# Kernel optimization log

Hardware: AMD Instinct MI355X
Metric: run time of the kernel (lower is better)

## Reference

```python
import jax, jax.numpy as jnp
import numpy as np

N = 8192; S = 32; EMB = 256; NH = 8; HD = EMB // NH; NT = 4; K = 2; L = 2; E = 131072
IN_DIMS = [128, 64, 32, 16]; COUNTS = [4096, 2048, 1024, 1024]
BETA = 1.0; TEMPER = 1.0; SLOPE = 0.2; LN_EPS = 1e-5


def setup_inputs() -> dict:
    key = jax.random.key(0)
    ks = iter(jax.random.split(key, 64))
    def nrm(shape, scale=1.0):
        return jax.random.normal(next(ks), shape, jnp.float32) * scale
    inp = {}
    for i, (d, c) in enumerate(zip(IN_DIMS, COUNTS)):
        inp[f"feat{i}"] = nrm((c, d))
        inp[f"Wfc{i}"] = nrm((d, EMB), d ** -0.5)
        inp[f"bfc{i}"] = nrm((EMB,), 0.01)
    inp["type_emb"] = nrm((NT, NT))
    inp["Wgcn"] = nrm((K, EMB, EMB), EMB ** -0.5)
    inp["bgcn"] = nrm((K, EMB), 0.01)
    inp["Wre"] = nrm((K, NT, NT), NT ** -0.5)
    inp["bre"] = nrm((K, NT), 0.01)
    inp["wtre"] = jnp.ones((K, NT), jnp.float32)
    inp["Wl"] = nrm((L, EMB, EMB), EMB ** -0.5)
    inp["Wr"] = nrm((L, EMB, EMB), EMB ** -0.5)
    inp["al"] = nrm((L, HD), HD ** -0.5)
    inp["ar"] = nrm((L, HD), HD ** -0.5)
    inp["Wrs"] = nrm((L, NT, NT * NH), NT ** -0.5)
    inp["Wrt"] = nrm((L, NT, NT * NH), NT ** -0.5)
    inp["Wfin"] = nrm((L, EMB, EMB), EMB ** -0.5)
    inp["ln_g"] = jnp.ones((L, EMB), jnp.float32)
    inp["ln_b"] = jnp.zeros((L, EMB), jnp.float32)
    inp["src"] = jax.random.randint(next(ks), (E,), 0, N)
    inp["dst"] = jax.random.randint(next(ks), (E,), 0, N)
    inp["node_type"] = jnp.concatenate([jnp.full((c,), t, jnp.int32) for t, c in enumerate(COUNTS)])
    inp["seqs"] = jax.random.randint(next(ks), (N, S), 0, N)
    return inp


def _l2n(x):
    return x / jnp.maximum(jnp.linalg.norm(x, axis=1, keepdims=True), 1e-12)


def _ln(x, g, b):
    m = x.mean(-1, keepdims=True)
    v = ((x - m) ** 2).mean(-1, keepdims=True)
    return (x - m) * jax.lax.rsqrt(v + LN_EPS) * g + b


def _agt(h, rh, Wl_, Wr_, al_, ar_, Wrs_, Wrt_, Wfin_, g_, b_):
    B, Sq, _ = h.shape
    fl = (h @ Wl_).reshape(B, Sq, NH, HD).transpose(0, 2, 1, 3)  # [B,NH,S,HD]
    fr = (h @ Wr_).reshape(B, Sq, NH, HD).transpose(0, 2, 1, 3)
    sl = jnp.einsum('bhsd,d->bhs', jax.nn.leaky_relu(fl, SLOPE), al_)
    sr = jnp.einsum('bhsd,d->bhs', jax.nn.leaky_relu(fr, SLOPE), ar_)
    score = sl[:, :, :, None] + sr[:, :, None, :]  # [B,NH,S,S]
    rk = (rh @ Wrs_).reshape(B, Sq, NH, NT).transpose(0, 2, 1, 3)  # [B,NH,S,NT]
    rq = (rh @ Wrt_).reshape(B, Sq, NH, NT).transpose(0, 2, 1, 3)
    score = score + BETA * jnp.einsum('bhir,bhjr->bhij', rk, rq)
    attn = jax.nn.softmax(score / TEMPER, axis=-1)
    ctx = jnp.einsum('bhij,bhjd->bhid', attn, fr)
    h_sa = ctx.transpose(0, 2, 1, 3).reshape(B, Sq, EMB)
    return _ln(h + h_sa @ Wfin_, g_, b_)


def reference(feat0, feat1, feat2, feat3, Wfc0, bfc0, Wfc1, bfc1, Wfc2, bfc2, Wfc3, bfc3,
              type_emb, Wgcn, bgcn, Wre, bre, wtre, Wl, Wr, al, ar, Wrs, Wrt, Wfin, ln_g, ln_b,
              src, dst, node_type, seqs):
    feats = [feat0, feat1, feat2, feat3]
    Wfcs = [Wfc0, Wfc1, Wfc2, Wfc3]
    bfcs = [bfc0, bfc1, bfc2, bfc3]
    gh = jnp.concatenate([f @ W + b for f, W, b in zip(feats, Wfcs, bfcs)], axis=0)  # [N,EMB]
    Nn = gh.shape[0]
    loop = jnp.arange(Nn, dtype=src.dtype)  # self-loops (graph.add_self_loop)
    src_f = jnp.concatenate([src, loop]); dst_f = jnp.concatenate([dst, loop])
    ones = jnp.ones(src_f.shape[0], jnp.float32)
    outdeg = jnp.clip(jax.ops.segment_sum(ones, src_f, num_segments=Nn), 1.0)
    indeg = jnp.clip(jax.ops.segment_sum(ones, dst_f, num_segments=Nn), 1.0)
    n_out = outdeg ** -0.5; n_in = indeg ** -0.5
    ret = [_l2n(gh)]
    R = type_emb[node_type]  # [N,NT]
    for k in range(K):
        # GraphConv, norm='both', relu
        x = (gh * n_out[:, None]) @ Wgcn[k]
        gh = jax.nn.relu(jax.ops.segment_sum(x[src_f], dst_f, num_segments=Nn) * n_in[:, None] + bgcn[k])
        # REConv: left norm, weight, per-node type scale, scatter-sum, right norm, bias, relu
        r = ((R * n_out[:, None]) @ Wre[k]) * wtre[k][node_type][:, None]
        R = jax.nn.relu(jax.ops.segment_sum(r[src_f], dst_f, num_segments=Nn) * n_in[:, None] + bre[k])
    h = gh[seqs]   # [N,S,EMB]
    rh = R[seqs]   # [N,S,NT]
    for l in range(L):
        h = _agt(h, rh, Wl[l], Wr[l], al[l], ar[l], Wrs[l], Wrt[l], Wfin[l], ln_g[l], ln_b[l])
        ret.append(_l2n(h[:, 0, :]))
    return jnp.concatenate(ret, axis=1)  # [N, EMB*(1+L)]
```

## Files before the change

kernel.cpp:

```cpp
#include <hip/hip_runtime.h>
#include <hip/hip_bf16.h>
#include <cstdint>
#include <cstddef>

typedef unsigned short ushortT;
typedef unsigned int uintT;

using bf16x8 = __attribute__((ext_vector_type(8))) short;
using f32x4  = __attribute__((ext_vector_type(4))) float;

static constexpr int NN  = 8192;
static constexpr int EE  = 131072;
static constexpr float SLOPE  = 0.2f;
static constexpr float LN_EPS = 1e-5f;

#define DEVI __device__ __forceinline__

DEVI float red32(float v) {
  #pragma unroll
  for (int m = 16; m >= 1; m >>= 1) v += __shfl_xor(v, m, 64);
  return v;
}
DEVI float red64(float v) {
  #pragma unroll
  for (int m = 32; m >= 1; m >>= 1) v += __shfl_xor(v, m, 64);
  return v;
}
DEVI float max32(float v) {
  #pragma unroll
  for (int m = 16; m >= 1; m >>= 1) v = fmaxf(v, __shfl_xor(v, m, 64));
  return v;
}
DEVI float blo(uintT u) { union { uintT i; float f; } c; c.i = u << 16; return c.f; }
DEVI float bhi(uintT u) { union { uintT i; float f; } c; c.i = u & 0xffff0000u; return c.f; }
DEVI float b2f(ushortT u) { union { uintT i; float f; } c; c.i = ((uintT)u) << 16; return c.f; }
DEVI ushortT f2bu(float f) {
  __hip_bfloat16 h = __float2bfloat16(f);
  return *reinterpret_cast<ushortT*>(&h);
}
DEVI void storeC(float* p, float v) { *p = v; }
DEVI void storeC(ushortT* p, float v) { *p = f2bu(v); }

__global__ __launch_bounds__(256) void fc_kernel(
    const float* __restrict__ f0, const float* __restrict__ f1,
    const float* __restrict__ f2, const float* __restrict__ f3,
    const float* __restrict__ w0, const float* __restrict__ w1,
    const float* __restrict__ w2, const float* __restrict__ w3,
    const float* __restrict__ b0, const float* __restrict__ b1,
    const float* __restrict__ b2, const float* __restrict__ b3,
    float* __restrict__ gh, float* __restrict__ out)
{
  const int nb = blockIdx.x * 32;
  const int t  = threadIdx.x;
  int base, D;
  const float *F, *W, *Bv;
  if (nb < 4096)      { base = 0;    D = 128; F = f0; W = w0; Bv = b0; }
  else if (nb < 6144) { base = 4096; D = 64;  F = f1; W = w1; Bv = b1; }
  else if (nb < 7168) { base = 6144; D = 32;  F = f2; W = w2; Bv = b2; }
  else                { base = 7168; D = 16;  F = f3; W = w3; Bv = b3; }

  __shared__ float Fs[32 * 128];
  __shared__ float red[32][4];
  __shared__ float nrm[32];

  const int total = 32 * D;
  for (int i = t; i < total; i += 256) Fs[i] = F[(size_t)(nb - base) * D + i];
  __syncthreads();

  float acc[32];
  #pragma unroll
  for (int r = 0; r < 32; ++r) acc[r] = Bv[t];
  for (int d = 0; d < D; ++d) {
    float w = W[(size_t)d * 256 + t];
    #pragma unroll
    for (int r = 0; r < 32; ++r) acc[r] = fmaf(Fs[r * D + d], w, acc[r]);
  }

  const int lane = t & 63, wid = t >> 6;
  #pragma unroll
  for (int r = 0; r < 32; ++r) {
    float v = acc[r] * acc[r];
    for (int o = 32; o > 0; o >>= 1) v += __shfl_down(v, o, 64);
    if (lane == 0) red[r][wid] = v;
  }
  __syncthreads();
  if (t < 32) {
    float s = red[t][0] + red[t][1] + red[t][2] + red[t][3];
    nrm[t] = 1.0f / fmaxf(sqrtf(s), 1e-12f);
  }
  __syncthreads();
  #pragma unroll
  for (int r = 0; r < 32; ++r) {
    gh[(size_t)(nb + r) * 256 + t]  = acc[r];
    out[(size_t)(nb + r) * 768 + t] = acc[r] * nrm[r];
  }
}

__global__ __launch_bounds__(256) void zero_counts(int* outc, int* inc) {
  int g = blockIdx.x * 256 + threadIdx.x;
  if (g < NN) outc[g] = 0; else inc[g - NN] = 0;
}
__global__ __launch_bounds__(256) void count_deg(const int* __restrict__ src,
                                                 const int* __restrict__ dst,
                                                 int* outc, int* inc) {
  int g = blockIdx.x * 256 + threadIdx.x;
  atomicAdd(&outc[src[g]], 1);
  atomicAdd(&inc[dst[g]], 1);
}
__global__ __launch_bounds__(256) void norm_kernel(const int* __restrict__ outc,
                                                   const int* __restrict__ inc,
                                                   float* n_out, float* n_in) {
  int g = blockIdx.x * 256 + threadIdx.x;
  n_out[g] = rsqrtf((float)outc[g] + 1.0f);
  n_in[g]  = rsqrtf((float)inc[g] + 1.0f);
}
__global__ __launch_bounds__(1024) void scan_kernel(const int* __restrict__ inc,
                                                    int* __restrict__ offs) {
  __shared__ int sums[1024];
  const int t = threadIdx.x;
  int x[8];
  const int base = t * 8;
  int s = 0;
  #pragma unroll
  for (int i = 0; i < 8; ++i) { int v = inc[base + i] + 1; x[i] = s; s += v; }
  sums[t] = s;
  __syncthreads();
  for (int off = 1; off < 1024; off <<= 1) {
    int a = (t >= off) ? sums[t - off] : 0;
    __syncthreads();
    sums[t] += a;
    __syncthreads();
  }
  const int pre = (t > 0) ? sums[t - 1] : 0;
  #pragma unroll
  for (int i = 0; i < 8; ++i) offs[base + i] = pre + x[i];
  if (t == 1023) offs[NN] = sums[1023];
}
__global__ __launch_bounds__(256) void copy_cur(const int* __restrict__ offs, int* cur) {
  int g = blockIdx.x * 256 + threadIdx.x;
  cur[g] = offs[g];
}
__global__ __launch_bounds__(256) void fill_csr(const int* __restrict__ src,
                                                const int* __restrict__ dst,
                                                int* cur, int* __restrict__ csr) {
  int g = blockIdx.x * 256 + threadIdx.x;
  int s, d;
  if (g < EE) { s = src[g]; d = dst[g]; }
  else        { s = g - EE; d = g - EE; }
  int pos = atomicAdd(&cur[d], 1);
  csr[pos] = s;
}
__global__ __launch_bounds__(256) void init_R(const float* __restrict__ type_emb,
                                              const int* __restrict__ nt,
                                              float* __restrict__ R) {
  int g = blockIdx.x * 256 + threadIdx.x;
  int n = g >> 2, c = g & 3;
  R[g] = type_emb[nt[n] * 4 + c];
}

template<bool ROWSCALE, bool STORE, bool RED, typename CT>
__global__ __launch_bounds__(256) void gemm64_kernel(
    const float* __restrict__ A,
    const float* __restrict__ W,
    const float* __restrict__ rowscale,
    CT* __restrict__ C,
    const float* __restrict__ avec,
    float* __restrict__ SSo)
{
  const int m0 = blockIdx.x * 64;
  const int n0 = blockIdx.y * 64;
  const int t  = threadIdx.x;
  const int tr = t & 15, tc = t >> 4;
  __shared__ alignas(16) float As[32][68];
  __shared__ alignas(16) float Bs[32][68];
  __shared__ float red[64][2];
  float acc[4][4] = {};

  for (int ks = 0; ks < 8; ++ks) {
    const int k0 = ks * 32;
    #pragma unroll
    for (int rep = 0; rep < 8; ++rep) {
      int flat = rep * 256 + t;
      int r = flat >> 5, c = flat & 31;
      As[c][r] = A[(size_t)(m0 + r) * 256 + (k0 + c)];
      int rb = flat >> 6, cb = flat & 63;
      Bs[rb][cb] = W[(size_t)(k0 + rb) * 256 + (n0 + cb)];
    }
    __syncthreads();
    #pragma unroll
    for (int k = 0; k < 32; ++k) {
      const float4 a4 = *reinterpret_cast<const float4*>(&As[k][tr * 4]);
      const float4 b4 = *reinterpret_cast<const float4*>(&Bs[k][tc * 4]);
      const float av[4] = {a4.x, a4.y, a4.z, a4.w};
      const float bv[4] = {b4.x, b4.y, b4.z, b4.w};
      #pragma unroll
      for (int u = 0; u < 4; ++u)
        #pragma unroll
        for (int v = 0; v < 4; ++v)
          acc[u][v] = fmaf(av[u], bv[v], acc[u][v]);
    }
    __syncthreads();
  }

  if constexpr (ROWSCALE) {
    #pragma unroll
    for (int u = 0; u < 4; ++u) {
      float s = rowscale[m0 + tr * 4 + u];
      #pragma unroll
      for (int v = 0; v < 4; ++v) acc[u][v] *= s;
    }
  }
  if constexpr (STORE) {
    #pragma unroll
    for (int u = 0; u < 4; ++u) {
      size_t row = (size_t)(m0 + tr * 4 + u);
      #pragma unroll
      for (int v = 0; v < 4; ++v)
        storeC(&C[row * 256 + (n0 + tc * 4 + v)], acc[u][v]);
    }
  }
  if constexpr (RED) {
    if (t < 128) red[t >> 1][t & 1] = 0.f;
    __syncthreads();
    #pragma unroll
    for (int u = 0; u < 4; ++u) {
      float s = 0.f;
      #pragma unroll
      for (int v = 0; v < 4; ++v) {
        float x = acc[u][v];
        float lr = x > 0.f ? x : SLOPE * x;
        s += lr * avec[(tc * 4 + v) & 31];
      }
      atomicAdd(&red[tr * 4 + u][tc >> 3], s);
    }
    __syncthreads();
    if (t < 128) {
      int r = t >> 1, hh = t & 1;
      SSo[(size_t)(m0 + r) * 8 + blockIdx.y * 2 + hh] = red[r][hh];
    }
  }
}

__global__ __launch_bounds__(256) void mfma_tab_kernel(
    const float* __restrict__ GR1, const float* __restrict__ gh,
    const float* __restrict__ Wfin, const float* __restrict__ Wc2,
    const float* __restrict__ Wcl, const float* __restrict__ Wg2,
    const float* __restrict__ Wgl2,
    ushortT* __restrict__ GWo, ushortT* __restrict__ GW2o,
    ushortT* __restrict__ GWLo, ushortT* __restrict__ GHGo,
    ushortT* __restrict__ GHLo)
{
  const int z = blockIdx.z;
  const float* A = (z < 3) ? GR1 : gh;
  const float* W = (z == 0) ? Wfin : (z == 1) ? Wc2 : (z == 2) ? Wcl
                 : (z == 3) ? Wg2 : Wgl2;
  ushortT* C = (z == 0) ? GWo : (z == 1) ? GW2o : (z == 2) ? GWLo
             : (z == 3) ? GHGo : GHLo;

  const int m0 = blockIdx.x * 64;
  const int n0 = blockIdx.y * 64;
  const int t = threadIdx.x;
  const int w = t >> 6, l = t & 63;
  const int wr = w >> 1, wc = w & 1;
  const int l15 = l & 15, l16 = l >> 4;

  __shared__ alignas(16) ushortT As[64][72];
  __shared__ alignas(16) ushortT Bs[64][72];

  f32x4 acc[2][2];
  #pragma unroll
  for (int mh = 0; mh < 2; ++mh)
    #pragma unroll
    for (int nh = 0; nh < 2; ++nh)
      #pragma unroll
      for (int r = 0; r < 4; ++r) acc[mh][nh][r] = 0.f;

  for (int k0 = 0; k0 < 256; k0 += 64) {
    #pragma unroll
    for (int rep = 0; rep < 16; ++rep) {
      int flat = rep * 256 + t;
      int r = flat >> 6, k = flat & 63;
      As[r][k] = f2bu(A[(size_t)(m0 + r) * 256 + k0 + k]);
    }
    #pragma unroll
    for (int rep = 0; rep < 16; ++rep) {
      int flat = rep * 256 + t;
      int k = flat >> 6, n = flat & 63;
      Bs[n][k] = f2bu(W[(size_t)(k0 + k) * 256 + n0 + n]);
    }
    __syncthreads();
    #pragma unroll
    for (int ks = 0; ks < 2; ++ks) {
      const int kb = ks * 32 + l16 * 8;
      bf16x8 afr[2], bfr[2];
      #pragma unroll
      for (int mh = 0; mh < 2; ++mh)
        afr[mh] = *reinterpret_cast<const bf16x8*>(&As[wr * 32 + mh * 16 + l15][kb]);
      #pragma unroll
      for (int nh = 0; nh < 2; ++nh)
        bfr[nh] = *reinterpret_cast<const bf16x8*>(&Bs[wc * 32 + nh * 16 + l15][kb]);
      #pragma unroll
      for (int mh = 0; mh < 2; ++mh)
        #pragma unroll
        for (int nh = 0; nh < 2; ++nh)
          acc[mh][nh] = __builtin_amdgcn_mfma_f32_16x16x32_bf16(
              afr[mh], bfr[nh], acc[mh][nh], 0, 0, 0);
    }
    __syncthreads();
  }
  #pragma unroll
  for (int mh = 0; mh < 2; ++mh)
    #pragma unroll
    for (int nh = 0; nh < 2; ++nh)
      #pragma unroll
      for (int r = 0; r < 4; ++r) {
        const int row = m0 + wr * 32 + mh * 16 + l16 * 4 + r;
        const int col = n0 + wc * 32 + nh * 16 + l15;
        C[(size_t)row * 256 + col] = f2bu(acc[mh][nh][r]);
      }
}

__global__ __launch_bounds__(256) void agg_kernel(
    const int* __restrict__ offs, const int* __restrict__ csr,
    const float* __restrict__ X, const float* __restrict__ n_in,
    const float* __restrict__ bias, float* __restrict__ ghn)
{
  const int n = blockIdx.x, t = threadIdx.x;
  const int s0 = offs[n], s1 = offs[n + 1];
  float acc = 0.f;
  for (int i = s0; i < s1; ++i) acc += X[(size_t)csr[i] * 256 + t];
  ghn[(size_t)n * 256 + t] = fmaxf(fmaf(acc, n_in[n], bias[t]), 0.f);
}
__global__ __launch_bounds__(256) void re_proj(
    const float* __restrict__ R, const float* __restrict__ n_out,
    const float* __restrict__ Wre, const float* __restrict__ wtre,
    const int* __restrict__ nt, float* __restrict__ rtmp)
{
  int g = blockIdx.x * 256 + threadIdx.x;
  int n = g >> 2, j = g & 3;
  float s = 0.f;
  #pragma unroll
  for (int c = 0; c < 4; ++c) s += R[n * 4 + c] * Wre[c * 4 + j];
  rtmp[g] = s * n_out[n] * wtre[nt[n]];
}
__global__ __launch_bounds__(256) void re_agg(
    const int* __restrict__ offs, const int* __restrict__ csr,
    const float* __restrict__ rtmp, const float* __restrict__ n_in,
    const float* __restrict__ bre, float* __restrict__ Rn)
{
  int g = blockIdx.x * 256 + threadIdx.x;
  int n = g >> 2, j = g & 3;
  float a = 0.f;
  for (int i = offs[n]; i < offs[n + 1]; ++i) a += rtmp[csr[i] * 4 + j];
  Rn[g] = fmaxf(fmaf(a, n_in[n], bre[j]), 0.f);
}
__global__ __launch_bounds__(256) void rkq_kernel(
    const float* __restrict__ R, const float* __restrict__ Wrs,
    const float* __restrict__ Wrt, float* __restrict__ RKQ)
{
  int g = blockIdx.x * 256 + threadIdx.x;
  int n = g >> 7, c = g & 127;
  int which = c >> 5, cc = c & 31;
  const float* Wp = (which == 0) ? Wrs : (which == 1) ? Wrt
                   : (which == 2) ? (Wrs + 128) : (Wrt + 128);
  float s = 0.f;
  #pragma unroll
  for (int r = 0; r < 4; ++r) s += R[n * 4 + r] * Wp[r * 32 + cc];
  RKQ[g] = s;
}

__global__ __launch_bounds__(256) void scale_w_kernel(
    const float* __restrict__ ln_g, const float* __restrict__ Wr2,
    const float* __restrict__ Wl2, float* __restrict__ Wg2,
    float* __restrict__ Wgl2)
{
  int g = blockIdx.x * 256 + threadIdx.x;
  float s = ln_g[g >> 8];
  Wg2[g]  = s * Wr2[g];
  Wgl2[g] = s * Wl2[g];
}
__global__ __launch_bounds__(256) void vec4_kernel(
    const float* __restrict__ ln_g, const float* __restrict__ ln_b,
    const float* __restrict__ Wr2, const float* __restrict__ Wl2,
    float* __restrict__ vecs)
{
  const int which = blockIdx.x, t = threadIdx.x;
  const float* W = (which < 2) ? Wr2 : Wl2;
  const float* s = (which & 1) ? ln_b : ln_g;
  float a = 0.f;
  for (int k = 0; k < 256; ++k) a = fmaf(s[k], W[(size_t)k * 256 + t], a);
  vecs[which * 256 + t] = a;
}

__global__ __launch_bounds__(256) void mega4_kernel(
    const int* __restrict__ seqs,
    const float* __restrict__ gh,
    const ushortT* __restrict__ GW, const ushortT* __restrict__ GW2,
    const ushortT* __restrict__ GWL, const ushortT* __restrict__ GHG,
    const ushortT* __restrict__ GHL,
    const float* __restrict__ SLg, const float* __restrict__ SRg,
    const float* __restrict__ RKQ,
    const float* __restrict__ vecs,
    const float* __restrict__ al2, const float* __restrict__ ar2,
    const float* __restrict__ ln_g, const float* __restrict__ ln_b,
    float* __restrict__ h1r0buf, float* __restrict__ ctx2buf,
    float* __restrict__ out)
{
  __shared__ int idx[32];
  __shared__ alignas(16) ushortT GT[256 * 40];
  __shared__ alignas(16) ushortT PlF[10240];
  __shared__ float SRs[8][32];
  __shared__ float RQs[32][36];
  __shared__ float rk2s[32];
  __shared__ float part[32][4], partq[32][4];
  __shared__ float mu_s[32], rs_s[32];
  __shared__ float SR2s[8][32];
  __shared__ float sl2s[8];
  __shared__ float scp[8][32];
  __shared__ float h1r0s[256];
  __shared__ float wred4[4];
  __shared__ float nrm1s;

  const int b = blockIdx.x, t = threadIdx.x;
  const int h8 = t >> 5, lo = t & 31;
  const int w = t >> 6, l = t & 63;
  const int l15 = l & 15, l16 = l >> 4;

  if (t < 32) idx[t] = seqs[b * 32 + t];
  __syncthreads();

  const float sli = SLg[(size_t)idx[lo] * 8 + h8];
  const float rk0 = RKQ[(size_t)idx[lo] * 128 + h8 * 4 + 0];
  const float rk1 = RKQ[(size_t)idx[lo] * 128 + h8 * 4 + 1];
  const float rk2_ = RKQ[(size_t)idx[lo] * 128 + h8 * 4 + 2];
  const float rk3 = RKQ[(size_t)idx[lo] * 128 + h8 * 4 + 3];

  {
    const uintT* GWu = reinterpret_cast<const uintT*>(GW);
    #pragma unroll
    for (int rep = 0; rep < 16; ++rep) {
      int flat = rep * 256 + t;
      int j = flat >> 7, cp = flat & 127;
      const uintT u = GWu[(size_t)idx[j] * 128 + cp];
      const int rA = 2 * cp;
      const int k = (rA >> 3) & 3;
      const int off = (((j >> 3) ^ k) << 3) + (j & 7);
      GT[rA * 40 + off]       = (ushortT)(u & 0xffffu);
      GT[(rA + 1) * 40 + off] = (ushortT)(u >> 16);
    }
  }
  SRs[h8][lo] = SRg[(size_t)idx[lo] * 8 + h8];
  #pragma unroll
  for (int rep = 0; rep < 4; ++rep) {
    int flat = rep * 256 + t, s3 = flat >> 5, c3 = flat & 31;
    RQs[s3][c3] = RKQ[(size_t)idx[s3] * 128 + 32 + c3];
  }
  if (t < 32) rk2s[t] = RKQ[(size_t)idx[0] * 128 + 64 + t];
  __syncthreads();

  {
    float p1[32];
    float m = -1e30f;
    #pragma unroll
    for (int j = 0; j < 32; ++j) {
      float sc = sli + SRs[h8][j]
               + rk0 * RQs[j][h8 * 4 + 0] + rk1 * RQs[j][h8 * 4 + 1]
               + rk2_ * RQs[j][h8 * 4 + 2] + rk3 * RQs[j][h8 * 4 + 3];
      p1[j] = sc; m = fmaxf(m, sc);
    }
    float sum = 0.f;
    #pragma unroll
    for (int j = 0; j < 32; ++j) { p1[j] = __expf(p1[j] - m); sum += p1[j]; }
    const float inv = 1.f / sum;
    const int row = t;
    const int k = (row >> 3) & 3;
    uintT* pw = reinterpret_cast<uintT*>(PlF);
    #pragma unroll
    for (int q = 0; q < 16; ++q) {
      const int pu = row * 20 + (((q >> 2) ^ k) << 2) + (q & 3);
      pw[pu] = (uintT)f2bu(p1[2 * q] * inv) | ((uintT)f2bu(p1[2 * q + 1] * inv) << 16);
    }
  }
  __syncthreads();

  int irow[2][4];
  #pragma unroll
  for (int mh = 0; mh < 2; ++mh)
    #pragma unroll
    for (int r = 0; r < 4; ++r)
      irow[mh][r] = idx[mh * 16 + l16 * 4 + r];

  bf16x8 af[2][2];
  #pragma unroll
  for (int hh = 0; hh < 2; ++hh) {
    const int h = 2 * w + hh;
    #pragma unroll
    for (int mh = 0; mh < 2; ++mh) {
      const int row = h * 32 + mh * 16 + l15;
      const int k = (row >> 3) & 3;
      af[hh][mh] = *reinterpret_cast<const bf16x8*>(&PlF[row * 40 + ((l16 ^ k) << 3)]);
    }
  }

  f32x4 acc[2][2][2];
  #pragma unroll
  for (int hh = 0; hh < 2; ++hh) {
    const int h = 2 * w + hh;
    bf16x8 bf[2];
    #pragma unroll
    for (int nh = 0; nh < 2; ++nh) {
      const int row = h * 32 + nh * 16 + l15;
      const int k = (row >> 3) & 3;
      bf[nh] = *reinterpret_cast<const bf16x8*>(&GT[row * 40 + ((l16 ^ k) << 3)]);
    }
    #pragma unroll
    for (int mh = 0; mh < 2; ++mh)
      #pragma unroll
      for (int nh = 0; nh < 2; ++nh) {
        f32x4 z = {0.f, 0.f, 0.f, 0.f};
        acc[hh][mh][nh] = __builtin_amdgcn_mfma_f32_16x16x32_bf16(af[hh][mh], bf[nh], z, 0, 0, 0);
      }
  }
  {
    float sum_[2][4], sq_[2][4];
    #pragma unroll
    for (int mh = 0; mh < 2; ++mh)
      #pragma unroll
      for (int r = 0; r < 4; ++r) { sum_[mh][r] = 0.f; sq_[mh][r] = 0.f; }
    #pragma unroll
    for (int hh = 0; hh < 2; ++hh)
      #pragma unroll
      for (int mh = 0; mh < 2; ++mh)
        #pragma unroll
        for (int nh = 0; nh < 2; ++nh) {
          const int col = (2 * w + hh) * 32 + nh * 16 + l15;
          #pragma unroll
          for (int r = 0; r < 4; ++r) {
            float v = acc[hh][mh][nh][r] + gh[(size_t)irow[mh][r] * 256 + col];
            acc[hh][mh][nh][r] = v;
            sum_[mh][r] += v;
            sq_[mh][r] = fmaf(v, v, sq_[mh][r]);
          }
        }
    #pragma unroll
    for (int mh = 0; mh < 2; ++mh)
      #pragma unroll
      for (int r = 0; r < 4; ++r) {
        float s = sum_[mh][r], q = sq_[mh][r];
        #pragma unroll
        for (int m = 8; m >= 1; m >>= 1) {
          s += __shfl_xor(s, m, 64);
          q += __shfl_xor(q, m, 64);
        }
        if (l15 == 0) {
          part[mh * 16 + l16 * 4 + r][w]  = s;
          partq[mh * 16 + l16 * 4 + r][w] = q;
        }
      }
    if (l16 == 0) {
      #pragma unroll
      for (int hh = 0; hh < 2; ++hh)
        #pragma unroll
        for (int nh = 0; nh < 2; ++nh)
          h1r0s[(2 * w + hh) * 32 + nh * 16 + l15] = acc[hh][0][nh][0];
    }
  }
  __syncthreads();

  if (t < 32) {
    float sm = part[t][0] + part[t][1] + part[t][2] + part[t][3];
    float sq = partq[t][0] + partq[t][1] + partq[t][2] + partq[t][3];
    const float m = sm * (1.f / 256.f);
    const float v = fmaxf(sq * (1.f / 256.f) - m * m, 0.f);
    mu_s[t] = m;
    rs_s[t] = rsqrtf(v + LN_EPS);
  }
  __syncthreads();

  {
    const uintT* GW2u = reinterpret_cast<const uintT*>(GW2);
    #pragma unroll
    for (int rep = 0; rep < 16; ++rep) {
      int flat = rep * 256 + t;
      int j = flat >> 7, cp = flat & 127;
      const uintT u = GW2u[(size_t)idx[j] * 128 + cp];
      const int rA = 2 * cp;
      const int k = (rA >> 3) & 3;
      const int off = (((j >> 3) ^ k) << 3) + (j & 7);
      GT[rA * 40 + off]       = (ushortT)(u & 0xffffu);
      GT[(rA + 1) * 40 + off] = (ushortT)(u >> 16);
    }
  }
  #pragma unroll
  for (int rep = 0; rep < 4; ++rep) {
    int flat = rep * 256 + t, s3 = flat >> 5, c3 = flat & 31;
    RQs[s3][c3] = RKQ[(size_t)idx[s3] * 128 + 96 + c3];
  }
  {
    const float mu0 = mu_s[0], rs0 = rs_s[0];
    float hv = fmaf((h1r0s[t] - mu0) * rs0, ln_g[t], ln_b[t]);
    h1r0buf[(size_t)b * 256 + t] = hv;
    float sq = red64(hv * hv);
    h1r0s[t] = hv;
    if ((t & 63) == 0) wred4[t >> 6] = sq;
  }
  {
    float z0 = 0.f;
    #pragma unroll 8
    for (int j = 0; j < 32; ++j)
      z0 = fmaf(b2f(PlF[(h8 * 32) * 40 + j]), b2f(GWL[(size_t)idx[j] * 256 + t]), z0);
    z0 += b2f(GHL[(size_t)idx[0] * 256 + t]);
    const float rs0 = rs_s[0], rm0 = rs_s[0] * mu_s[0];
    const float fl = fmaf(rs0, z0, fmaf(-rm0, vecs[512 + t], vecs[768 + t]));
    float lr = (fl > 0.f ? fl : SLOPE * fl) * al2[lo];
    lr = red32(lr);
    if (lo == 0) sl2s[h8] = lr;
  }
  __syncthreads();

  if (t == 0) nrm1s = 1.f / fmaxf(sqrtf(wred4[0] + wred4[1] + wred4[2] + wred4[3]), 1e-12f);

  {
    f32x4 acc2[2][2][2];
    #pragma unroll
    for (int hh = 0; hh < 2; ++hh) {
      const int h = 2 * w + hh;
      bf16x8 bf[2];
      #pragma unroll
      for (int nh = 0; nh < 2; ++nh) {
        const int row = h * 32 + nh * 16 + l15;
        const int k = (row >> 3) & 3;
        bf[nh] = *reinterpret_cast<const bf16x8*>(&GT[row * 40 + ((l16 ^ k) << 3)]);
      }
      #pragma unroll
      for (int mh = 0; mh < 2; ++mh)
        #pragma unroll
        for (int nh = 0; nh < 2; ++nh) {
          f32x4 z = {0.f, 0.f, 0.f, 0.f};
          acc2[hh][mh][nh] = __builtin_amdgcn_mfma_f32_16x16x32_bf16(af[hh][mh], bf[nh], z, 0, 0, 0);
        }
    }
    float rsv[2][4], rmv[2][4];
    #pragma unroll
    for (int mh = 0; mh < 2; ++mh)
      #pragma unroll
      for (int r = 0; r < 4; ++r) {
        const int row = mh * 16 + l16 * 4 + r;
        rsv[mh][r] = rs_s[row];
        rmv[mh][r] = rsv[mh][r] * mu_s[row];
      }
    float ar2v[2] = { ar2[l15], ar2[16 + l15] };
    float v1c[2][2], v2c[2][2];
    #pragma unroll
    for (int hh = 0; hh < 2; ++hh)
      #pragma unroll
      for (int nh = 0; nh < 2; ++nh) {
        const int col = (2 * w + hh) * 32 + nh * 16 + l15;
        v1c[hh][nh] = vecs[col];
        v2c[hh][nh] = vecs[256 + col];
      }
    float sacc[2][2][4];
    #pragma unroll
    for (int hh = 0; hh < 2; ++hh)
      #pragma unroll
      for (int mh = 0; mh < 2; ++mh)
        #pragma unroll
        for (int r = 0; r < 4; ++r) sacc[hh][mh][r] = 0.f;

    #pragma unroll
    for (int hh = 0; hh < 2; ++hh)
      #pragma unroll
      for (int mh = 0; mh < 2; ++mh)
        #pragma unroll
        for (int nh = 0; nh < 2; ++nh) {
          const int col = (2 * w + hh) * 32 + nh * 16 + l15;
          #pragma unroll
          for (int r = 0; r < 4; ++r) {
            const int row = mh * 16 + l16 * 4 + r;
            float yv = acc2[hh][mh][nh][r] + b2f(GHG[(size_t)irow[mh][r] * 256 + col]);
            float fa = fmaf(rsv[mh][r], yv, fmaf(-rmv[mh][r], v1c[hh][nh], v2c[hh][nh]));
            PlF[row * 268 + col] = f2bu(fa);
            float lr = fa > 0.f ? fa : SLOPE * fa;
            sacc[hh][mh][r] = fmaf(lr, ar2v[nh], sacc[hh][mh][r]);
          }
        }
    #pragma unroll
    for (int hh = 0; hh < 2; ++hh)
      #pragma unroll
      for (int mh = 0; mh < 2; ++mh)
        #pragma unroll
        for (int r = 0; r < 4; ++r) {
          float s = sacc[hh][mh][r];
          #pragma unroll
          for (int m = 8; m >= 1; m >>= 1) s += __shfl_xor(s, m, 64);
          if (l15 == 0) SR2s[2 * w + hh][mh * 16 + l16 * 4 + r] = s;
        }
  }
  __syncthreads();

  {
    float s2 = sl2s[h8] + SR2s[h8][lo]
             + rk2s[h8 * 4 + 0] * RQs[lo][h8 * 4 + 0]
             + rk2s[h8 * 4 + 1] * RQs[lo][h8 * 4 + 1]
             + rk2s[h8 * 4 + 2] * RQs[lo][h8 * 4 + 2]
             + rk2s[h8 * 4 + 3] * RQs[lo][h8 * 4 + 3];
    const float m2 = max32(s2);
    const float e = __expf(s2 - m2);
    const float su = red32(e);
    scp[h8][lo] = e / su;
  }
  __syncthreads();

  {
    float a = 0.f;
    #pragma unroll
    for (int j = 0; j < 32; ++j) a = fmaf(scp[h8][j], b2f(PlF[j * 268 + t]), a);
    ctx2buf[(size_t)b * 256 + t] = a;
  }
  out[(size_t)b * 768 + 256 + t] = h1r0s[t] * nrm1s;
}

__global__ __launch_bounds__(256) void final_ln_kernel(
    const float* __restrict__ A,
    const float* __restrict__ W,
    const float* __restrict__ res,
    const float* __restrict__ lng, const float* __restrict__ lnb,
    float* __restrict__ out)
{
  const int m0 = blockIdx.x * 64;
  const int t  = threadIdx.x;
  const int tr = t & 15, tc = t >> 4;
  __shared__ alignas(16) float As[32][68];
  __shared__ alignas(16) float Bs[32][264];
  __shared__ float red[64][16];
  __shared__ float stat[64];
  float acc[4][16] = {};

  for (int ks = 0; ks < 8; ++ks) {
    const int k0 = ks * 32;
    #pragma unroll
    for (int rep = 0; rep < 8; ++rep) {
      int flat = rep * 256 + t;
      int r = flat >> 5, c = flat & 31;
      As[c][r] = A[(size_t)(m0 + r) * 256 + (k0 + c)];
    }
    #pragma unroll
    for (int rep = 0; rep < 32; ++rep) {
      int flat = rep * 256 + t;
      int rb = flat >> 8, cb = flat & 255;
      Bs[rb][cb] = W[(size_t)(k0 + rb) * 256 + cb];
    }
    __syncthreads();
    #pragma unroll
    for (int k = 0; k < 32; ++k) {
      const float4 a4 = *reinterpret_cast<const float4*>(&As[k][tr * 4]);
      const float av[4] = {a4.x, a4.y, a4.z, a4.w};
      #pragma unroll
      for (int q = 0; q < 4; ++q) {
        const float4 b4 = *reinterpret_cast<const float4*>(&Bs[k][tc * 16 + q * 4]);
        const float bv[4] = {b4.x, b4.y, b4.z, b4.w};
        #pragma unroll
        for (int u = 0; u < 4; ++u)
          #pragma unroll
          for (int v = 0; v < 4; ++v)
            acc[u][q * 4 + v] = fmaf(av[u], bv[v], acc[u][q * 4 + v]);
      }
    }
    __syncthreads();
  }

  int rows[4];
  #pragma unroll
  for (int u = 0; u < 4; ++u) rows[u] = m0 + tr * 4 + u;

  #pragma unroll
  for (int u = 0; u < 4; ++u) {
    const float* rp = &res[(size_t)rows[u] * 256 + tc * 16];
    #pragma unroll
    for (int v = 0; v < 16; ++v) acc[u][v] += rp[v];
  }
  #pragma unroll
  for (int u = 0; u < 4; ++u) {
    float s = 0.f;
    #pragma unroll
    for (int v = 0; v < 16; ++v) s += acc[u][v];
    red[tr * 4 + u][tc] = s;
  }
  __syncthreads();
  if (t < 64) {
    float s = 0.f;
    #pragma unroll
    for (int g = 0; g < 16; ++g) s += red[t][g];
    stat[t] = s * (1.0f / 256.0f);
  }
  __syncthreads();
  float mu[4];
  #pragma unroll
  for (int u = 0; u < 4; ++u) mu[u] = stat[tr * 4 + u];
  #pragma unroll
  for (int u = 0; u < 4; ++u) {
    float s = 0.f;
    #pragma unroll
    for (int v = 0; v < 16; ++v) { float d = acc[u][v] - mu[u]; s += d * d; }
    red[tr * 4 + u][tc] = s;
  }
  __syncthreads();
  if (t < 64) {
    float s = 0.f;
    #pragma unroll
    for (int g = 0; g < 16; ++g) s += red[t][g];
    stat[t] = rsqrtf(s * (1.0f / 256.0f) + LN_EPS);
  }
  __syncthreads();
  float rst[4];
  #pragma unroll
  for (int u = 0; u < 4; ++u) rst[u] = stat[tr * 4 + u];
  #pragma unroll
  for (int u = 0; u < 4; ++u) {
    float s = 0.f;
    #pragma unroll
    for (int v = 0; v < 16; ++v) {
      int col = tc * 16 + v;
      float yv = fmaf((acc[u][v] - mu[u]) * rst[u], lng[col], lnb[col]);
      acc[u][v] = yv;
      s += yv * yv;
    }
    red[tr * 4 + u][tc] = s;
  }
  __syncthreads();
  if (t < 64) {
    float s = 0.f;
    #pragma unroll
    for (int g = 0; g < 16; ++g) s += red[t][g];
    stat[t] = 1.0f / fmaxf(sqrtf(s), 1e-12f);
  }
  __syncthreads();
  #pragma unroll
  for (int u = 0; u < 4; ++u) {
    float rn = stat[tr * 4 + u];
    #pragma unroll
    for (int v = 0; v < 16; ++v)
      out[(size_t)rows[u] * 768 + 512 + tc * 16 + v] = acc[u][v] * rn;
  }
}

extern "C" void kernel_launch(void* const* d_in, const int* in_sizes, int n_in,
                              void* d_out, int out_size, void* d_ws, size_t ws_size,
                              hipStream_t stream)
{
  (void)in_sizes; (void)n_in; (void)out_size; (void)ws_size;

  const float* feat[4]; const float* wfc[4]; const float* bfc[4];
  for (int i = 0; i < 4; ++i) {
    feat[i] = (const float*)d_in[i * 3 + 0];
    wfc[i]  = (const float*)d_in[i * 3 + 1];
    bfc[i]  = (const float*)d_in[i * 3 + 2];
  }
  const float* type_emb = (const float*)d_in[12];
  const float* Wgcn = (const float*)d_in[13];
  const float* bgcn = (const float*)d_in[14];
  const float* Wre  = (const float*)d_in[15];
  const float* bre  = (const float*)d_in[16];
  const float* wtre = (const float*)d_in[17];
  const float* Wl   = (const float*)d_in[18];
  const float* Wr   = (const float*)d_in[19];
  const float* al   = (const float*)d_in[20];
  const float* ar   = (const float*)d_in[21];
  const float* Wrs  = (const float*)d_in[22];
  const float* Wrt  = (const float*)d_in[23];
  const float* Wfin = (const float*)d_in[24];
  const float* ln_g = (const float*)d_in[25];
  const float* ln_b = (const float*)d_in[26];
  const int* src       = (const int*)d_in[27];
  const int* dst       = (const int*)d_in[28];
  const int* node_type = (const int*)d_in[29];
  const int* seqs      = (const int*)d_in[30];
  float* out = (float*)d_out;

  char* p = (char*)d_ws;
  auto take = [&](size_t n) { char* q = p; p += (n + 255) & ~(size_t)255; return q; };
  float* gh    = (float*)take((size_t)NN * 256 * 4);
  float* Xbuf  = (float*)take((size_t)NN * 256 * 4);
  float* GR1   = (float*)take((size_t)NN * 256 * 4);
  float* RKQ   = (float*)take((size_t)NN * 128 * 4);
  float* SLg   = (float*)take((size_t)NN * 8 * 4);
  float* SRg   = (float*)take((size_t)NN * 8 * 4);
  float* n_out = (float*)take((size_t)NN * 4);
  float* n_in_ = (float*)take((size_t)NN * 4);
  int*   outc  = (int*)take((size_t)NN * 4);
  int*   inc   = (int*)take((size_t)NN * 4);
  int*   offs  = (int*)take((size_t)(NN + 1) * 4);
  int*   cur   = (int*)take((size_t)NN * 4);
  int*   csr   = (int*)take((size_t)(EE + NN) * 4);
  float* R     = (float*)take((size_t)NN * 4 * 4);
  float* rtmp  = (float*)take((size_t)NN * 4 * 4);
  ushortT* GW  = (ushortT*)take((size_t)NN * 256 * 2);
  ushortT* GW2 = (ushortT*)take((size_t)NN * 256 * 2);
  ushortT* GWL = (ushortT*)take((size_t)NN * 256 * 2);
  ushortT* GHG = (ushortT*)take((size_t)NN * 256 * 2);
  ushortT* GHL = (ushortT*)take((size_t)NN * 256 * 2);
  float* Wg2   = (float*)take((size_t)65536 * 4);
  float* Wgl2  = (float*)take((size_t)65536 * 4);
  float* Wc2   = (float*)take((size_t)65536 * 4);
  float* Wcl   = (float*)take((size_t)65536 * 4);
  float* vecs  = (float*)take((size_t)4 * 256 * 4);
  float* ctx2buf = Xbuf;
  float* h1r0buf = GR1;

  const float* Wr2 = Wr + 65536;
  const float* Wl2 = Wl + 65536;

  fc_kernel<<<256, 256, 0, stream>>>(feat[0], feat[1], feat[2], feat[3],
                                     wfc[0], wfc[1], wfc[2], wfc[3],
                                     bfc[0], bfc[1], bfc[2], bfc[3], gh, out);
  zero_counts<<<64, 256, 0, stream>>>(outc, inc);
  count_deg<<<512, 256, 0, stream>>>(src, dst, outc, inc);
  norm_kernel<<<32, 256, 0, stream>>>(outc, inc, n_out, n_in_);
  scan_kernel<<<1, 1024, 0, stream>>>(inc, offs);
  copy_cur<<<32, 256, 0, stream>>>(offs, cur);
  fill_csr<<<544, 256, 0, stream>>>(src, dst, cur, csr);
  init_R<<<128, 256, 0, stream>>>(type_emb, node_type, R);

  scale_w_kernel<<<256, 256, 0, stream>>>(ln_g, Wr2, Wl2, Wg2, Wgl2);
  vec4_kernel<<<4, 256, 0, stream>>>(ln_g, ln_b, Wr2, Wl2, vecs);
  gemm64_kernel<false, true, false, float>
      <<<dim3(4, 4), 256, 0, stream>>>(Wfin, Wg2, nullptr, Wc2, nullptr, nullptr);
  gemm64_kernel<false, true, false, float>
      <<<dim3(4, 4), 256, 0, stream>>>(Wfin, Wgl2, nullptr, Wcl, nullptr, nullptr);

  for (int k = 0; k < 2; ++k) {
    gemm64_kernel<true, true, false, float>
        <<<dim3(128, 4), 256, 0, stream>>>(gh, Wgcn + (size_t)k * 65536,
                                           n_out, Xbuf, nullptr, nullptr);
    agg_kernel<<<NN, 256, 0, stream>>>(offs, csr, Xbuf, n_in_, bgcn + k * 256, gh);
    re_proj<<<128, 256, 0, stream>>>(R, n_out, Wre + k * 16, wtre + k * 4, node_type, rtmp);
    re_agg<<<128, 256, 0, stream>>>(offs, csr, rtmp, n_in_, bre + k * 4, R);
  }

  rkq_kernel<<<4096, 256, 0, stream>>>(R, Wrs, Wrt, RKQ);
  gemm64_kernel<false, false, true, float>
      <<<dim3(128, 4), 256, 0, stream>>>(gh, Wl, nullptr, (float*)nullptr, al, SLg);
  gemm64_kernel<false, true, true, float>
      <<<dim3(128, 4), 256, 0, stream>>>(gh, Wr, nullptr, GR1, ar, SRg);
  mfma_tab_kernel<<<dim3(128, 4, 5), 256, 0, stream>>>(
      GR1, gh, Wfin, Wc2, Wcl, Wg2, Wgl2, GW, GW2, GWL, GHG, GHL);

  mega4_kernel<<<NN, 256, 0, stream>>>(seqs, gh, GW, GW2, GWL, GHG, GHL,
                                       SLg, SRg, RKQ, vecs,
                                       al + 32, ar + 32, ln_g, ln_b,
                                       h1r0buf, ctx2buf, out);

  final_ln_kernel<<<128, 256, 0, stream>>>(ctx2buf, Wfin + 65536, h1r0buf,
                                           ln_g + 256, ln_b + 256, out);
}
```

Measured before the change: 627.2 us.

## Compute layer-2 projection per sequence in-kernel instead of precomputed per-node tables

Drops the five precomputed per-node bf16 tables (GW2, GWL, GHG, GHL and the weight products Wc2/Wcl). The mega kernel now builds the layer-1 output tile in shared memory and multiplies it by a transposed, ln_g-scaled bf16 Wr2 through MFMA. The left-score path becomes a direct 256x256 dot product of h1r0 with a bf16 Wl2. gh is read as a bf16 copy. This removes four 8192x256 table GEMMs and the matching gather traffic, but adds per-block MFMA work (32x256x256), weight reads from global or L2, extra bf16 rounding of the residual and of h1, and a serial 256-length loop per thread.

Result: faster. 604.7 us (-3.6%).

```diff
diff --git a/kernel.cpp b/kernel.cpp
--- a/kernel.cpp
+++ b/kernel.cpp
@@ -242,21 +242,9 @@
 }
 
 __global__ __launch_bounds__(256) void mfma_tab_kernel(
-    const float* __restrict__ GR1, const float* __restrict__ gh,
-    const float* __restrict__ Wfin, const float* __restrict__ Wc2,
-    const float* __restrict__ Wcl, const float* __restrict__ Wg2,
-    const float* __restrict__ Wgl2,
-    ushortT* __restrict__ GWo, ushortT* __restrict__ GW2o,
-    ushortT* __restrict__ GWLo, ushortT* __restrict__ GHGo,
-    ushortT* __restrict__ GHLo)
-{
-  const int z = blockIdx.z;
-  const float* A = (z < 3) ? GR1 : gh;
-  const float* W = (z == 0) ? Wfin : (z == 1) ? Wc2 : (z == 2) ? Wcl
-                 : (z == 3) ? Wg2 : Wgl2;
-  ushortT* C = (z == 0) ? GWo : (z == 1) ? GW2o : (z == 2) ? GWLo
-             : (z == 3) ? GHGo : GHLo;
-
+    const float* __restrict__ A, const float* __restrict__ W,
+    ushortT* __restrict__ C)
+{
   const int m0 = blockIdx.x * 64;
   const int n0 = blockIdx.y * 64;
   const int t = threadIdx.x;
@@ -369,46 +357,49 @@
   RKQ[g] = s;
 }
 
-__global__ __launch_bounds__(256) void scale_w_kernel(
-    const float* __restrict__ ln_g, const float* __restrict__ Wr2,
-    const float* __restrict__ Wl2, float* __restrict__ Wg2,
-    float* __restrict__ Wgl2)
-{
-  int g = blockIdx.x * 256 + threadIdx.x;
-  float s = ln_g[g >> 8];
-  Wg2[g]  = s * Wr2[g];
-  Wgl2[g] = s * Wl2[g];
-}
 __global__ __launch_bounds__(256) void vec4_kernel(
     const float* __restrict__ ln_g, const float* __restrict__ ln_b,
-    const float* __restrict__ Wr2, const float* __restrict__ Wl2,
-    float* __restrict__ vecs)
+    const float* __restrict__ Wr2, float* __restrict__ vecs)
 {
   const int which = blockIdx.x, t = threadIdx.x;
-  const float* W = (which < 2) ? Wr2 : Wl2;
   const float* s = (which & 1) ? ln_b : ln_g;
   float a = 0.f;
-  for (int k = 0; k < 256; ++k) a = fmaf(s[k], W[(size_t)k * 256 + t], a);
+  for (int k = 0; k < 256; ++k) a = fmaf(s[k], Wr2[(size_t)k * 256 + t], a);
   vecs[which * 256 + t] = a;
 }
-
-__global__ __launch_bounds__(256) void mega4_kernel(
+__global__ __launch_bounds__(256) void wg2t_kernel(
+    const float* __restrict__ ln_g, const float* __restrict__ Wr2,
+    const float* __restrict__ Wl2,
+    ushortT* __restrict__ Wg2T, ushortT* __restrict__ Wl2b)
+{
+  const int c = blockIdx.x, t = threadIdx.x;
+  Wg2T[(size_t)c * 256 + t] = f2bu(ln_g[t] * Wr2[(size_t)t * 256 + c]);
+  Wl2b[(size_t)c * 256 + t] = f2bu(Wl2[(size_t)c * 256 + t]);
+}
+__global__ __launch_bounds__(256) void ghb_kernel(
+    const float* __restrict__ gh, ushortT* __restrict__ ghb)
+{
+  int g = blockIdx.x * 256 + threadIdx.x;
+  ghb[g] = f2bu(gh[g]);
+}
+
+__global__ __launch_bounds__(256) void mega5_kernel(
     const int* __restrict__ seqs,
-    const float* __restrict__ gh,
-    const ushortT* __restrict__ GW, const ushortT* __restrict__ GW2,
-    const ushortT* __restrict__ GWL, const ushortT* __restrict__ GHG,
-    const ushortT* __restrict__ GHL,
+    const ushortT* __restrict__ ghb,
+    const ushortT* __restrict__ GW,
     const float* __restrict__ SLg, const float* __restrict__ SRg,
     const float* __restrict__ RKQ,
     const float* __restrict__ vecs,
+    const ushortT* __restrict__ Wg2T,
+    const ushortT* __restrict__ Wl2b,
     const float* __restrict__ al2, const float* __restrict__ ar2,
     const float* __restrict__ ln_g, const float* __restrict__ ln_b,
     float* __restrict__ h1r0buf, float* __restrict__ ctx2buf,
     float* __restrict__ out)
 {
   __shared__ int idx[32];
-  __shared__ alignas(16) ushortT GT[256 * 40];
-  __shared__ alignas(16) ushortT PlF[10240];
+  __shared__ alignas(16) ushortT bufA[10240];
+  __shared__ alignas(16) ushortT bufB[10240];
   __shared__ float SRs[8][32];
   __shared__ float RQs[32][36];
   __shared__ float rk2s[32];
@@ -445,8 +436,8 @@
       const int rA = 2 * cp;
       const int k = (rA >> 3) & 3;
       const int off = (((j >> 3) ^ k) << 3) + (j & 7);
-      GT[rA * 40 + off]       = (ushortT)(u & 0xffffu);
-      GT[(rA + 1) * 40 + off] = (ushortT)(u >> 16);
+      bufA[rA * 40 + off]       = (ushortT)(u & 0xffffu);
+      bufA[(rA + 1) * 40 + off] = (ushortT)(u >> 16);
     }
   }
   SRs[h8][lo] = SRg[(size_t)idx[lo] * 8 + h8];
@@ -474,7 +465,7 @@
     const float inv = 1.f / sum;
     const int row = t;
     const int k = (row >> 3) & 3;
-    uintT* pw = reinterpret_cast<uintT*>(PlF);
+    uintT* pw = reinterpret_cast<uintT*>(bufB);
     #pragma unroll
     for (int q = 0; q < 16; ++q) {
       const int pu = row * 20 + (((q >> 2) ^ k) << 2) + (q & 3);
@@ -498,7 +489,7 @@
     for (int mh = 0; mh < 2; ++mh) {
       const int row = h * 32 + mh * 16 + l15;
       const int k = (row >> 3) & 3;
-      af[hh][mh] = *reinterpret_cast<const bf16x8*>(&PlF[row * 40 + ((l16 ^ k) << 3)]);
+      af[hh][mh] = *reinterpret_cast<const bf16x8*>(&bufB[row * 40 + ((l16 ^ k) << 3)]);
     }
   }
 
@@ -511,7 +502,7 @@
     for (int nh = 0; nh < 2; ++nh) {
       const int row = h * 32 + nh * 16 + l15;
       const int k = (row >> 3) & 3;
-      bf[nh] = *reinterpret_cast<const bf16x8*>(&GT[row * 40 + ((l16 ^ k) << 3)]);
+      bf[nh] = *reinterpret_cast<const bf16x8*>(&bufA[row * 40 + ((l16 ^ k) << 3)]);
     }
     #pragma unroll
     for (int mh = 0; mh < 2; ++mh)
@@ -536,7 +527,7 @@
           const int col = (2 * w + hh) * 32 + nh * 16 + l15;
           #pragma unroll
           for (int r = 0; r < 4; ++r) {
-            float v = acc[hh][mh][nh][r] + gh[(size_t)irow[mh][r] * 256 + col];
+            float v = acc[hh][mh][nh][r] + b2f(ghb[(size_t)irow[mh][r] * 256 + col]);
             acc[hh][mh][nh][r] = v;
             sum_[mh][r] += v;
             sq_[mh][r] = fmaf(v, v, sq_[mh][r]);
@@ -577,20 +568,19 @@
   }
   __syncthreads();
 
-  {
-    const uintT* GW2u = reinterpret_cast<const uintT*>(GW2);
-    #pragma unroll
-    for (int rep = 0; rep < 16; ++rep) {
-      int flat = rep * 256 + t;
-      int j = flat >> 7, cp = flat & 127;
-      const uintT u = GW2u[(size_t)idx[j] * 128 + cp];
-      const int rA = 2 * cp;
-      const int k = (rA >> 3) & 3;
-      const int off = (((j >> 3) ^ k) << 3) + (j & 7);
-      GT[rA * 40 + off]       = (ushortT)(u & 0xffffu);
-      GT[(rA + 1) * 40 + off] = (ushortT)(u >> 16);
-    }
-  }
+  #pragma unroll
+  for (int hh = 0; hh < 2; ++hh)
+    #pragma unroll
+    for (int mh = 0; mh < 2; ++mh)
+      #pragma unroll
+      for (int nh = 0; nh < 2; ++nh) {
+        const int col = (2 * w + hh) * 32 + nh * 16 + l15;
+        #pragma unroll
+        for (int r = 0; r < 4; ++r) {
+          const int row = mh * 16 + l16 * 4 + r;
+          bufB[row * 264 + col] = f2bu(acc[hh][mh][nh][r]);
+        }
+      }
   #pragma unroll
   for (int rep = 0; rep < 4; ++rep) {
     int flat = rep * 256 + t, s3 = flat >> 5, c3 = flat & 31;
@@ -604,41 +594,33 @@
     h1r0s[t] = hv;
     if ((t & 63) == 0) wred4[t >> 6] = sq;
   }
+  __syncthreads();
+
+  if (t == 0) nrm1s = 1.f / fmaxf(sqrtf(wred4[0] + wred4[1] + wred4[2] + wred4[3]), 1e-12f);
+
   {
-    float z0 = 0.f;
-    #pragma unroll 8
-    for (int j = 0; j < 32; ++j)
-      z0 = fmaf(b2f(PlF[(h8 * 32) * 40 + j]), b2f(GWL[(size_t)idx[j] * 256 + t]), z0);
-    z0 += b2f(GHL[(size_t)idx[0] * 256 + t]);
-    const float rs0 = rs_s[0], rm0 = rs_s[0] * mu_s[0];
-    const float fl = fmaf(rs0, z0, fmaf(-rm0, vecs[512 + t], vecs[768 + t]));
-    float lr = (fl > 0.f ? fl : SLOPE * fl) * al2[lo];
-    lr = red32(lr);
-    if (lo == 0) sl2s[h8] = lr;
-  }
-  __syncthreads();
-
-  if (t == 0) nrm1s = 1.f / fmaxf(sqrtf(wred4[0] + wred4[1] + wred4[2] + wred4[3]), 1e-12f);
-
-  {
-    f32x4 acc2[2][2][2];
-    #pragma unroll
-    for (int hh = 0; hh < 2; ++hh) {
-      const int h = 2 * w + hh;
-      bf16x8 bf[2];
-      #pragma unroll
-      for (int nh = 0; nh < 2; ++nh) {
-        const int row = h * 32 + nh * 16 + l15;
-        const int k = (row >> 3) & 3;
-        bf[nh] = *reinterpret_cast<const bf16x8*>(&GT[row * 40 + ((l16 ^ k) << 3)]);
+    f32x4 acc2[2][4];
+    #pragma unroll
+    for (int mh = 0; mh < 2; ++mh)
+      #pragma unroll
+      for (int cg = 0; cg < 4; ++cg)
+        #pragma unroll
+        for (int r = 0; r < 4; ++r) acc2[mh][cg][r] = 0.f;
+    #pragma unroll
+    for (int ks = 0; ks < 8; ++ks) {
+      const int ko = ks * 32 + l16 * 8;
+      bf16x8 a2[2];
+      #pragma unroll
+      for (int mh = 0; mh < 2; ++mh)
+        a2[mh] = *reinterpret_cast<const bf16x8*>(&bufB[(mh * 16 + l15) * 264 + ko]);
+      #pragma unroll
+      for (int cg = 0; cg < 4; ++cg) {
+        const int col = w * 64 + cg * 16 + l15;
+        bf16x8 b2 = *reinterpret_cast<const bf16x8*>(&Wg2T[(size_t)col * 256 + ko]);
+        #pragma unroll
+        for (int mh = 0; mh < 2; ++mh)
+          acc2[mh][cg] = __builtin_amdgcn_mfma_f32_16x16x32_bf16(a2[mh], b2, acc2[mh][cg], 0, 0, 0);
       }
-      #pragma unroll
-      for (int mh = 0; mh < 2; ++mh)
-        #pragma unroll
-        for (int nh = 0; nh < 2; ++nh) {
-          f32x4 z = {0.f, 0.f, 0.f, 0.f};
-          acc2[hh][mh][nh] = __builtin_amdgcn_mfma_f32_16x16x32_bf16(af[hh][mh], bf[nh], z, 0, 0, 0);
-        }
     }
     float rsv[2][4], rmv[2][4];
     #pragma unroll
@@ -649,41 +631,30 @@
         rsv[mh][r] = rs_s[row];
         rmv[mh][r] = rsv[mh][r] * mu_s[row];
       }
+    float sacc[2][2][4];
+    #pragma unroll
+    for (int hh = 0; hh < 2; ++hh)
+      #pragma unroll
+      for (int mh = 0; mh < 2; ++mh)
+        #pragma unroll
+        for (int r = 0; r < 4; ++r) sacc[hh][mh][r] = 0.f;
     float ar2v[2] = { ar2[l15], ar2[16 + l15] };
-    float v1c[2][2], v2c[2][2];
-    #pragma unroll
-    for (int hh = 0; hh < 2; ++hh)
-      #pragma unroll
-      for (int nh = 0; nh < 2; ++nh) {
-        const int col = (2 * w + hh) * 32 + nh * 16 + l15;
-        v1c[hh][nh] = vecs[col];
-        v2c[hh][nh] = vecs[256 + col];
-      }
-    float sacc[2][2][4];
-    #pragma unroll
-    for (int hh = 0; hh < 2; ++hh)
+    #pragma unroll
+    for (int cg = 0; cg < 4; ++cg) {
+      const int col = w * 64 + cg * 16 + l15;
+      const float v1c = vecs[col], v2c = vecs[256 + col];
+      const int hh = cg >> 1;
       #pragma unroll
       for (int mh = 0; mh < 2; ++mh)
         #pragma unroll
-        for (int r = 0; r < 4; ++r) sacc[hh][mh][r] = 0.f;
-
-    #pragma unroll
-    for (int hh = 0; hh < 2; ++hh)
-      #pragma unroll
-      for (int mh = 0; mh < 2; ++mh)
-        #pragma unroll
-        for (int nh = 0; nh < 2; ++nh) {
-          const int col = (2 * w + hh) * 32 + nh * 16 + l15;
-          #pragma unroll
-          for (int r = 0; r < 4; ++r) {
-            const int row = mh * 16 + l16 * 4 + r;
-            float yv = acc2[hh][mh][nh][r] + b2f(GHG[(size_t)irow[mh][r] * 256 + col]);
-            float fa = fmaf(rsv[mh][r], yv, fmaf(-rmv[mh][r], v1c[hh][nh], v2c[hh][nh]));
-            PlF[row * 268 + col] = f2bu(fa);
-            float lr = fa > 0.f ? fa : SLOPE * fa;
-            sacc[hh][mh][r] = fmaf(lr, ar2v[nh], sacc[hh][mh][r]);
-          }
+        for (int r = 0; r < 4; ++r) {
+          const int row = mh * 16 + l16 * 4 + r;
+          float fa = fmaf(rsv[mh][r], acc2[mh][cg][r], fmaf(-rmv[mh][r], v1c, v2c));
+          bufA[row * 268 + col] = f2bu(fa);
+          float lr = fa > 0.f ? fa : SLOPE * fa;
+          sacc[hh][mh][r] = fmaf(lr, ar2v[cg & 1], sacc[hh][mh][r]);
         }
+    }
     #pragma unroll
     for (int hh = 0; hh < 2; ++hh)
       #pragma unroll
@@ -695,6 +666,15 @@
           for (int m = 8; m >= 1; m >>= 1) s += __shfl_xor(s, m, 64);
           if (l15 == 0) SR2s[2 * w + hh][mh * 16 + l16 * 4 + r] = s;
         }
+  }
+  {
+    float fl = 0.f;
+    #pragma unroll 8
+    for (int k = 0; k < 256; ++k)
+      fl = fmaf(h1r0s[k], b2f(Wl2b[(size_t)k * 256 + t]), fl);
+    float lr = (fl > 0.f ? fl : SLOPE * fl) * al2[lo];
+    lr = red32(lr);
+    if (lo == 0) sl2s[h8] = lr;
   }
   __syncthreads();
 
@@ -714,7 +694,7 @@
   {
     float a = 0.f;
     #pragma unroll
-    for (int j = 0; j < 32; ++j) a = fmaf(scp[h8][j], b2f(PlF[j * 268 + t]), a);
+    for (int j = 0; j < 32; ++j) a = fmaf(scp[h8][j], b2f(bufA[j * 268 + t]), a);
     ctx2buf[(size_t)b * 256 + t] = a;
   }
   out[(size_t)b * 768 + 256 + t] = h1r0s[t] * nrm1s;
@@ -894,16 +874,11 @@
   int*   csr   = (int*)take((size_t)(EE + NN) * 4);
   float* R     = (float*)take((size_t)NN * 4 * 4);
   float* rtmp  = (float*)take((size_t)NN * 4 * 4);
-  ushortT* GW  = (ushortT*)take((size_t)NN * 256 * 2);
-  ushortT* GW2 = (ushortT*)take((size_t)NN * 256 * 2);
-  ushortT* GWL = (ushortT*)take((size_t)NN * 256 * 2);
-  ushortT* GHG = (ushortT*)take((size_t)NN * 256 * 2);
-  ushortT* GHL = (ushortT*)take((size_t)NN * 256 * 2);
-  float* Wg2   = (float*)take((size_t)65536 * 4);
-  float* Wgl2  = (float*)take((size_t)65536 * 4);
-  float* Wc2   = (float*)take((size_t)65536 * 4);
-  float* Wcl   = (float*)take((size_t)65536 * 4);
-  float* vecs  = (float*)take((size_t)4 * 256 * 4);
+  ushortT* GW   = (ushortT*)take((size_t)NN * 256 * 2);
+  ushortT* ghb  = (ushortT*)take((size_t)NN * 256 * 2);
+  ushortT* Wg2T = (ushortT*)take((size_t)65536 * 2);
+  ushortT* Wl2b = (ushortT*)take((size_t)65536 * 2);
+  float* vecs  = (float*)take((size_t)2 * 256 * 4);
   float* ctx2buf = Xbuf;
   float* h1r0buf = GR1;
 
@@ -921,12 +896,8 @@
   fill_csr<<<544, 256, 0, stream>>>(src, dst, cur, csr);
   init_R<<<128, 256, 0, stream>>>(type_emb, node_type, R);
 
-  scale_w_kernel<<<256, 256, 0, stream>>>(ln_g, Wr2, Wl2, Wg2, Wgl2);
-  vec4_kernel<<<4, 256, 0, stream>>>(ln_g, ln_b, Wr2, Wl2, vecs);
-  gemm64_kernel<false, true, false, float>
-      <<<dim3(4, 4), 256, 0, stream>>>(Wfin, Wg2, nullptr, Wc2, nullptr, nullptr);
-  gemm64_kernel<false, true, false, float>
-      <<<dim3(4, 4), 256, 0, stream>>>(Wfin, Wgl2, nullptr, Wcl, nullptr, nullptr);
+  vec4_kernel<<<2, 256, 0, stream>>>(ln_g, ln_b, Wr2, vecs);
+  wg2t_kernel<<<256, 256, 0, stream>>>(ln_g, Wr2, Wl2, Wg2T, Wl2b);
 
   for (int k = 0; k < 2; ++k) {
     gemm64_kernel<true, true, false, float>
@@ -942,11 +913,11 @@
       <<<dim3(128, 4), 256, 0, stream>>>(gh, Wl, nullptr, (float*)nullptr, al, SLg);
   gemm64_kernel<false, true, true, float>
       <<<dim3(128, 4), 256, 0, stream>>>(gh, Wr, nullptr, GR1, ar, SRg);
-  mfma_tab_kernel<<<dim3(128, 4, 5), 256, 0, stream>>>(
-      GR1, gh, Wfin, Wc2, Wcl, Wg2, Wgl2, GW, GW2, GWL, GHG, GHL);
-
-  mega4_kernel<<<NN, 256, 0, stream>>>(seqs, gh, GW, GW2, GWL, GHG, GHL,
-                                       SLg, SRg, RKQ, vecs,
+  mfma_tab_kernel<<<dim3(128, 4), 256, 0, stream>>>(GR1, Wfin, GW);
+  ghb_kernel<<<NN, 256, 0, stream>>>(gh, ghb);
+
+  mega5_kernel<<<NN, 256, 0, stream>>>(seqs, ghb, GW, SLg, SRg, RKQ, vecs,
+                                       Wg2T, Wl2b,
                                        al + 32, ar + 32, ln_g, ln_b,
                                        h1r0buf, ctx2buf, out);
 
```
